# Performance work log

Hardware: AMD Instinct MI355X
Metric: run time of the kernel (lower is better)

The kernel has to match this reference:

```python
import jax, jax.numpy as jnp
import numpy as np

B, N = 2048, 64
D, H = 64, 256
CARD_V, UNIT_V, ENEMY_V, AT_V, SRC_V, MODE_V, TER_V, SITE_V, SKILL_V = 400, 100, 120, 50, 30, 10, 12, 25, 60
STATE_SC, CE_SC, SITE_SC, ME_SC, ACT_SC = 64, 8, 6, 8, 16
L_HAND, L_UNIT, L_CE, L_SK, L_VS, L_ME, L_TGT = 16, 8, 8, 8, 16, 16, 8
STATE_IN = STATE_SC + 6 * D + (D + CE_SC) + (D + SITE_SC) + (D + ME_SC)  # 662
ACT_IN = 7 * D + ACT_SC  # 464


def setup_inputs() -> dict:
    key = jax.random.key(0)
    ks = iter(jax.random.split(key, 64))
    nrm = lambda shape, s=1.0: jax.random.normal(next(ks), shape, jnp.float32) * s
    ri = lambda shape, hi: jax.random.randint(next(ks), shape, 0, hi, jnp.int32)
    return {
        'state_scalars': nrm((B, STATE_SC)),
        'mode_id': ri((B,), MODE_V), 'terrain_id': ri((B,), TER_V), 'site_type_id': ri((B,), SITE_V),
        'hand_ids': ri((B, L_HAND), CARD_V), 'hand_mask': ri((B, L_HAND), 2),
        'unit_ids': ri((B, L_UNIT), UNIT_V), 'unit_mask': ri((B, L_UNIT), 2),
        'combat_enemy_ids': ri((B, L_CE), ENEMY_V), 'combat_enemy_scalars': nrm((B, L_CE, CE_SC)), 'combat_enemy_mask': ri((B, L_CE), 2),
        'skill_ids': ri((B, L_SK), SKILL_V), 'skill_mask': ri((B, L_SK), 2),
        'visible_site_ids': ri((B, L_VS), SITE_V), 'visible_site_scalars': nrm((B, L_VS, SITE_SC)), 'visible_site_mask': ri((B, L_VS), 2),
        'map_enemy_ids': ri((B, L_ME), ENEMY_V), 'map_enemy_scalars': nrm((B, L_ME, ME_SC)), 'map_enemy_mask': ri((B, L_ME), 2),
        'action_ids': ri((B, N, 6), SRC_V),  # SRC_V=30 is min over the 6 id vocabs -> always in range
        'action_scalars': nrm((B, N, ACT_SC)),
        'target_enemy_ids': ri((B, N, L_TGT), ENEMY_V), 'target_mask': ri((B, N, L_TGT), 2),
        'card_emb': nrm((CARD_V, D), 0.05), 'unit_emb': nrm((UNIT_V, D), 0.05), 'enemy_emb': nrm((ENEMY_V, D), 0.05),
        'action_type_emb': nrm((AT_V, D), 0.05), 'source_emb': nrm((SRC_V, D), 0.05), 'mode_emb': nrm((MODE_V, D), 0.05),
        'terrain_emb': nrm((TER_V, D), 0.05), 'site_emb': nrm((SITE_V, D), 0.05), 'skill_emb': nrm((SKILL_V, D), 0.05),
        'map_site_emb': nrm((SITE_V, D), 0.05),
        'W_s': nrm((STATE_IN, H), 0.02), 'b_s': jnp.zeros((H,), jnp.float32),
        'W_a': nrm((ACT_IN, H), 0.02), 'b_a': jnp.zeros((H,), jnp.float32),
        'W1': nrm((2 * H, H), 0.02), 'b1': jnp.zeros((H,), jnp.float32),
        'W2': nrm((H, 1), 0.02), 'b2': jnp.zeros((1,), jnp.float32),
        'W_v': nrm((H, 1), 0.02), 'b_v': jnp.zeros((1,), jnp.float32),
    }


def masked_mean(x, mask):
    # x: [..., L, D'], mask: [..., L] (0/1). Empty list -> zeros (count clamped to 1).
    m = mask.astype(x.dtype)[..., None]
    s = jnp.sum(x * m, axis=-2)
    c = jnp.maximum(jnp.sum(m, axis=-2), 1.0)
    return s / c


def reference(state_scalars, mode_id, terrain_id, site_type_id, hand_ids, hand_mask,
              unit_ids, unit_mask, combat_enemy_ids, combat_enemy_scalars, combat_enemy_mask,
              skill_ids, skill_mask, visible_site_ids, visible_site_scalars, visible_site_mask,
              map_enemy_ids, map_enemy_scalars, map_enemy_mask, action_ids, action_scalars,
              target_enemy_ids, target_mask, card_emb, unit_emb, enemy_emb, action_type_emb,
              source_emb, mode_emb, terrain_emb, site_emb, skill_emb, map_site_emb,
              W_s, b_s, W_a, b_a, W1, b1, W2, b2, W_v, b_v):
    # ---- state encoding (batched version of encode_state) ----
    hand_pool = masked_mean(card_emb[hand_ids], hand_mask)            # [B, D]
    unit_pool = masked_mean(unit_emb[unit_ids], unit_mask)            # [B, D]
    ce = jnp.concatenate([enemy_emb[combat_enemy_ids], combat_enemy_scalars], axis=-1)
    ce_pool = masked_mean(ce, combat_enemy_mask)                      # [B, D+CE_SC]
    skill_pool = masked_mean(skill_emb[skill_ids], skill_mask)        # [B, D]
    vs = jnp.concatenate([map_site_emb[visible_site_ids], visible_site_scalars], axis=-1)
    vs_pool = masked_mean(vs, visible_site_mask)                      # [B, D+SITE_SC]
    me = jnp.concatenate([enemy_emb[map_enemy_ids], map_enemy_scalars], axis=-1)
    me_pool = masked_mean(me, map_enemy_mask)                         # [B, D+ME_SC]
    state_input = jnp.concatenate([
        state_scalars, mode_emb[mode_id], hand_pool, unit_pool,
        terrain_emb[terrain_id], site_emb[site_type_id],
        ce_pool, skill_pool, vs_pool, me_pool], axis=-1)              # [B, 662]
    state_repr = jnp.tanh(state_input @ W_s + b_s)                    # [B, H]
    # ---- action encoding (batched encode_actions) ----
    tgt_pool = masked_mean(enemy_emb[target_enemy_ids], target_mask)  # [B, N, D]
    action_input = jnp.concatenate([
        action_type_emb[action_ids[..., 0]], source_emb[action_ids[..., 1]],
        card_emb[action_ids[..., 2]], unit_emb[action_ids[..., 3]],
        enemy_emb[action_ids[..., 4]], skill_emb[action_ids[..., 5]],
        tgt_pool, action_scalars], axis=-1)                           # [B, N, 464]
    action_reprs = jnp.tanh(action_input @ W_a + b_a)                 # [B, N, H]
    # ---- scoring + value heads ----
    state_b = jnp.broadcast_to(state_repr[:, None, :], (state_repr.shape[0], action_reprs.shape[1], state_repr.shape[1]))
    combined = jnp.concatenate([state_b, action_reprs], axis=-1)      # [B, N, 2H]
    logits = (jnp.tanh(combined @ W1 + b1) @ W2 + b2)[..., 0]         # [B, N]
    value = (state_repr @ W_v + b_v)[..., 0]                          # [B]
    return logits, value
```

## Files before the change

kernel.cpp:

```cpp
#include <hip/hip_runtime.h>
#include <hip/hip_bf16.h>

#define BB 2048
#define NN 64
#define DD 64
#define HH 256
#define L_HAND 16
#define L_UNIT 8
#define L_CE 8
#define L_SK 8
#define L_VS 16
#define L_ME 16
#define L_TGT 8
#define STATE_SC 64
#define CE_SC 8
#define SITE_SC 6
#define ME_SC 8
#define ACT_SC 16
#define STATE_IN 662
#define ACT_IN 464

#define SROWS 2
#define SK 672
#define SSTRIDE 676

typedef __attribute__((ext_vector_type(8))) short short8;
typedef __attribute__((ext_vector_type(4))) float f32x4;

__device__ __forceinline__ float fast_tanh(float x) {
    float e = __expf(2.0f * x);
    return 1.0f - 2.0f * __builtin_amdgcn_rcpf(e + 1.0f);
}
__device__ __forceinline__ short f2bs(float x) {
    __hip_bfloat16 h = __float2bfloat16(x);
    return *reinterpret_cast<short*>(&h);
}
__device__ __forceinline__ float bs2f(short u) {
    union { unsigned int i; float f; } v;
    v.i = ((unsigned int)(unsigned short)u) << 16;
    return v.f;
}
__device__ __forceinline__ void async_copy16(const void* gsrc, void* ldst) {
    __builtin_amdgcn_global_load_lds(
        (const __attribute__((address_space(1))) unsigned int*)gsrc,
        (__attribute__((address_space(3))) unsigned int*)ldst, 16, 0, 0);
}
__device__ __forceinline__ float sum16_dpp(float v) {
    int x;
    x = __builtin_amdgcn_update_dpp(0, __float_as_int(v), 0x111, 0xf, 0xf, true);
    v += __int_as_float(x);
    x = __builtin_amdgcn_update_dpp(0, __float_as_int(v), 0x112, 0xf, 0xf, true);
    v += __int_as_float(x);
    x = __builtin_amdgcn_update_dpp(0, __float_as_int(v), 0x114, 0xf, 0xf, true);
    v += __int_as_float(x);
    x = __builtin_amdgcn_update_dpp(0, __float_as_int(v), 0x118, 0xf, 0xf, true);
    v += __int_as_float(x);
    return v;
}

#define RO_AT    0
#define RO_SRC   50
#define RO_CARD  80
#define RO_UNIT  480
#define RO_ENEMY 580
#define RO_SKILL 700
#define EMB_ROWS 760

#define T0 (480 * 256)
#define T1 (T0 + 256 * 256)
#define T2 (T1 + EMB_ROWS * 64)
#define T3 (T2 + SK * 256)
#define T4 (T3 + 256 * 256)

__global__ __launch_bounds__(256) void pack_kernel(
    const float* __restrict__ W_a, const float* __restrict__ W1,
    const float* __restrict__ W_s,
    const float* __restrict__ at_emb, const float* __restrict__ src_emb,
    const float* __restrict__ card_emb, const float* __restrict__ unit_emb,
    const float* __restrict__ enemy_emb, const float* __restrict__ skill_emb,
    ushort* __restrict__ WaP, ushort* __restrict__ W1bP, ushort* __restrict__ emb16,
    ushort* __restrict__ WsP, ushort* __restrict__ W1aP)
{
    const int idx = blockIdx.x * 256 + threadIdx.x;
    if (idx < T0) {
        const int k = idx >> 8, n = idx & 255;
        const float v = (k < ACT_IN) ? W_a[k * HH + n] : 0.f;
        const int pi = (((k >> 5) * 16 + (n >> 4)) * 64 +
                        ((n & 15) + 16 * ((k >> 3) & 3))) * 8 + (k & 7);
        WaP[pi] = (ushort)f2bs(v);
    } else if (idx < T1) {
        const int j = idx - T0;
        const int k = j >> 8, n = j & 255;
        const float v = W1[(256 + k) * HH + n];
        const int pi = (((k >> 5) * 16 + (n >> 4)) * 64 +
                        ((n & 15) + 16 * ((k >> 3) & 3))) * 8 + (k & 7);
        W1bP[pi] = (ushort)f2bs(v);
    } else if (idx < T2) {
        const int j = idx - T1;
        const int row = j >> 6, d = j & 63;
        float v;
        if      (row < RO_SRC)   v = at_emb[row * 64 + d];
        else if (row < RO_CARD)  v = src_emb[(row - RO_SRC) * 64 + d];
        else if (row < RO_UNIT)  v = card_emb[(row - RO_CARD) * 64 + d];
        else if (row < RO_ENEMY) v = unit_emb[(row - RO_UNIT) * 64 + d];
        else if (row < RO_SKILL) v = enemy_emb[(row - RO_ENEMY) * 64 + d];
        else                     v = skill_emb[(row - RO_SKILL) * 64 + d];
        emb16[j] = (ushort)f2bs(v);
    } else if (idx < T3) {
        const int j = idx - T2;
        const int k = j >> 8, n = j & 255;
        const float v = (k < STATE_IN) ? W_s[k * HH + n] : 0.f;
        const int pi = (((k >> 5) * 16 + (n >> 4)) * 64 +
                        ((n & 15) + 16 * ((k >> 3) & 3))) * 8 + (k & 7);
        WsP[pi] = (ushort)f2bs(v);
    } else if (idx < T4) {
        const int j = idx - T3;
        const int k = j >> 8, n = j & 255;
        const float v = W1[k * HH + n];
        const int pi = (((k >> 5) * 16 + (n >> 4)) * 64 +
                        ((n & 15) + 16 * ((k >> 3) & 3))) * 8 + (k & 7);
        W1aP[pi] = (ushort)f2bs(v);
    }
}

__global__ __launch_bounds__(256) void state_mfma_kernel(
    const float* __restrict__ state_scalars,
    const int* __restrict__ mode_id, const int* __restrict__ terrain_id,
    const int* __restrict__ site_type_id,
    const int* __restrict__ hand_ids, const int* __restrict__ hand_mask,
    const int* __restrict__ unit_ids, const int* __restrict__ unit_mask,
    const int* __restrict__ ce_ids, const float* __restrict__ ce_sc, const int* __restrict__ ce_mask,
    const int* __restrict__ skill_ids, const int* __restrict__ skill_mask,
    const int* __restrict__ vs_ids, const float* __restrict__ vs_sc, const int* __restrict__ vs_mask,
    const int* __restrict__ me_ids, const float* __restrict__ me_sc, const int* __restrict__ me_mask,
    const float* __restrict__ mode_emb, const float* __restrict__ ter_emb,
    const float* __restrict__ site_emb, const float* __restrict__ msite_emb,
    const ushort* __restrict__ emb16,
    const ushort* __restrict__ WsP, const float* __restrict__ b_s,
    const ushort* __restrict__ W1aP,
    const float* __restrict__ W_v, const float* __restrict__ b_v,
    float* __restrict__ s_part, float* __restrict__ out_value)
{
    __shared__ float s_in[SROWS * SSTRIDE];
    __shared__ ushort sA2[8 * 64 * 8];
    __shared__ float red[4][4];

    const int t = threadIdx.x;
    const int b0 = blockIdx.x * SROWS;
    const int w = t >> 6;
    const int lane = t & 63;
    const ushort* card16  = emb16 + RO_CARD  * 64;
    const ushort* unit16  = emb16 + RO_UNIT  * 64;
    const ushort* enemy16 = emb16 + RO_ENEMY * 64;
    const ushort* skill16 = emb16 + RO_SKILL * 64;

    for (int u = t; u < SROWS * 84; u += 256) {
        const int r  = u / 84;
        const int un = u - r * 84;
        const int b  = b0 + r;
        float* dst = s_in + r * SSTRIDE;
        if (un < 8) {
            const int o0 = un * 8;
            const float4 f0 = *(const float4*)(state_scalars + b * STATE_SC + o0);
            const float4 f1 = *(const float4*)(state_scalars + b * STATE_SC + o0 + 4);
            *(float4*)(dst + o0) = f0; *(float4*)(dst + o0 + 4) = f1;
        } else if (un < 16) {
            const int d0 = (un - 8) * 8;
            const float4 f0 = *(const float4*)(mode_emb + mode_id[b] * DD + d0);
            const float4 f1 = *(const float4*)(mode_emb + mode_id[b] * DD + d0 + 4);
            *(float4*)(dst + 64 + d0) = f0; *(float4*)(dst + 64 + d0 + 4) = f1;
        } else if (un < 24) {
            const int d0 = (un - 16) * 8;
            float acc[8] = {0,0,0,0,0,0,0,0}; int c = 0;
#pragma unroll
            for (int l = 0; l < L_HAND; ++l) {
                const int mk = hand_mask[b * L_HAND + l]; c += mk;
                const float fm = (float)mk;
                const short8 e = *(const short8*)(card16 + hand_ids[b * L_HAND + l] * 64 + d0);
#pragma unroll
                for (int q = 0; q < 8; ++q) acc[q] = fmaf(fm, bs2f(e[q]), acc[q]);
            }
            const float inv = 1.0f / (float)(c > 1 ? c : 1);
#pragma unroll
            for (int q = 0; q < 8; ++q) dst[128 + d0 + q] = acc[q] * inv;
        } else if (un < 32) {
            const int d0 = (un - 24) * 8;
            float acc[8] = {0,0,0,0,0,0,0,0}; int c = 0;
#pragma unroll
            for (int l = 0; l < L_UNIT; ++l) {
                const int mk = unit_mask[b * L_UNIT + l]; c += mk;
                const float fm = (float)mk;
                const short8 e = *(const short8*)(unit16 + unit_ids[b * L_UNIT + l] * 64 + d0);
#pragma unroll
                for (int q = 0; q < 8; ++q) acc[q] = fmaf(fm, bs2f(e[q]), acc[q]);
            }
            const float inv = 1.0f / (float)(c > 1 ? c : 1);
#pragma unroll
            for (int q = 0; q < 8; ++q) dst[192 + d0 + q] = acc[q] * inv;
        } else if (un < 40) {
            const int d0 = (un - 32) * 8;
            const float4 f0 = *(const float4*)(ter_emb + terrain_id[b] * DD + d0);
            const float4 f1 = *(const float4*)(ter_emb + terrain_id[b] * DD + d0 + 4);
            *(float4*)(dst + 256 + d0) = f0; *(float4*)(dst + 256 + d0 + 4) = f1;
        } else if (un < 48) {
            const int d0 = (un - 40) * 8;
            const float4 f0 = *(const float4*)(site_emb + site_type_id[b] * DD + d0);
            const float4 f1 = *(const float4*)(site_emb + site_type_id[b] * DD + d0 + 4);
            *(float4*)(dst + 320 + d0) = f0; *(float4*)(dst + 320 + d0 + 4) = f1;
        } else if (un < 56) {
            const int d0 = (un - 48) * 8;
            float acc[8] = {0,0,0,0,0,0,0,0}; int c = 0;
#pragma unroll
            for (int l = 0; l < L_CE; ++l) {
                const int mk = ce_mask[b * L_CE + l]; c += mk;
                const float fm = (float)mk;
                const short8 e = *(const short8*)(enemy16 + ce_ids[b * L_CE + l] * 64 + d0);
#pragma unroll
                for (int q = 0; q < 8; ++q) acc[q] = fmaf(fm, bs2f(e[q]), acc[q]);
            }
            const float inv = 1.0f / (float)(c > 1 ? c : 1);
#pragma unroll
            for (int q = 0; q < 8; ++q) dst[384 + d0 + q] = acc[q] * inv;
        } else if (un == 56) {
            float acc[8] = {0,0,0,0,0,0,0,0}; int c = 0;
#pragma unroll
            for (int l = 0; l < L_CE; ++l) {
                const int mk = ce_mask[b * L_CE + l]; c += mk;
                const float fm = (float)mk;
                const float4 f0 = *(const float4*)(ce_sc + (b * L_CE + l) * CE_SC);
                const float4 f1 = *(const float4*)(ce_sc + (b * L_CE + l) * CE_SC + 4);
                acc[0] = fmaf(fm, f0.x, acc[0]); acc[1] = fmaf(fm, f0.y, acc[1]);
                acc[2] = fmaf(fm, f0.z, acc[2]); acc[3] = fmaf(fm, f0.w, acc[3]);
                acc[4] = fmaf(fm, f1.x, acc[4]); acc[5] = fmaf(fm, f1.y, acc[5]);
                acc[6] = fmaf(fm, f1.z, acc[6]); acc[7] = fmaf(fm, f1.w, acc[7]);
            }
            const float inv = 1.0f / (float)(c > 1 ? c : 1);
#pragma unroll
            for (int q = 0; q < 8; ++q) dst[448 + q] = acc[q] * inv;
        } else if (un < 65) {
            const int d0 = (un - 57) * 8;
            float acc[8] = {0,0,0,0,0,0,0,0}; int c = 0;
#pragma unroll
            for (int l = 0; l < L_SK; ++l) {
                const int mk = skill_mask[b * L_SK + l]; c += mk;
                const float fm = (float)mk;
                const short8 e = *(const short8*)(skill16 + skill_ids[b * L_SK + l] * 64 + d0);
#pragma unroll
                for (int q = 0; q < 8; ++q) acc[q] = fmaf(fm, bs2f(e[q]), acc[q]);
            }
            const float inv = 1.0f / (float)(c > 1 ? c : 1);
#pragma unroll
            for (int q = 0; q < 8; ++q) dst[456 + d0 + q] = acc[q] * inv;
        } else if (un < 73) {
            const int d0 = (un - 65) * 8;
            float acc[8] = {0,0,0,0,0,0,0,0}; int c = 0;
#pragma unroll
            for (int l = 0; l < L_VS; ++l) {
                const int mk = vs_mask[b * L_VS + l]; c += mk;
                const float fm = (float)mk;
                const float4 f0 = *(const float4*)(msite_emb + vs_ids[b * L_VS + l] * DD + d0);
                const float4 f1 = *(const float4*)(msite_emb + vs_ids[b * L_VS + l] * DD + d0 + 4);
                acc[0] = fmaf(fm, f0.x, acc[0]); acc[1] = fmaf(fm, f0.y, acc[1]);
                acc[2] = fmaf(fm, f0.z, acc[2]); acc[3] = fmaf(fm, f0.w, acc[3]);
                acc[4] = fmaf(fm, f1.x, acc[4]); acc[5] = fmaf(fm, f1.y, acc[5]);
                acc[6] = fmaf(fm, f1.z, acc[6]); acc[7] = fmaf(fm, f1.w, acc[7]);
            }
            const float inv = 1.0f / (float)(c > 1 ? c : 1);
#pragma unroll
            for (int q = 0; q < 8; ++q) dst[520 + d0 + q] = acc[q] * inv;
        } else if (un == 73) {
            float acc[6] = {0,0,0,0,0,0}; int c = 0;
#pragma unroll
            for (int l = 0; l < L_VS; ++l) {
                const int mk = vs_mask[b * L_VS + l]; c += mk;
                const float fm = (float)mk;
                const float* p = vs_sc + (b * L_VS + l) * SITE_SC;
#pragma unroll
                for (int q = 0; q < 6; ++q) acc[q] = fmaf(fm, p[q], acc[q]);
            }
            const float inv = 1.0f / (float)(c > 1 ? c : 1);
#pragma unroll
            for (int q = 0; q < 6; ++q) dst[584 + q] = acc[q] * inv;
        } else if (un < 82) {
            const int d0 = (un - 74) * 8;
            float acc[8] = {0,0,0,0,0,0,0,0}; int c = 0;
#pragma unroll
            for (int l = 0; l < L_ME; ++l) {
                const int mk = me_mask[b * L_ME + l]; c += mk;
                const float fm = (float)mk;
                const short8 e = *(const short8*)(enemy16 + me_ids[b * L_ME + l] * 64 + d0);
#pragma unroll
                for (int q = 0; q < 8; ++q) acc[q] = fmaf(fm, bs2f(e[q]), acc[q]);
            }
            const float inv = 1.0f / (float)(c > 1 ? c : 1);
#pragma unroll
            for (int q = 0; q < 8; ++q) dst[590 + d0 + q] = acc[q] * inv;
        } else if (un == 82) {
            float acc[8] = {0,0,0,0,0,0,0,0}; int c = 0;
#pragma unroll
            for (int l = 0; l < L_ME; ++l) {
                const int mk = me_mask[b * L_ME + l]; c += mk;
                const float fm = (float)mk;
                const float4 f0 = *(const float4*)(me_sc + (b * L_ME + l) * ME_SC);
                const float4 f1 = *(const float4*)(me_sc + (b * L_ME + l) * ME_SC + 4);
                acc[0] = fmaf(fm, f0.x, acc[0]); acc[1] = fmaf(fm, f0.y, acc[1]);
                acc[2] = fmaf(fm, f0.z, acc[2]); acc[3] = fmaf(fm, f0.w, acc[3]);
                acc[4] = fmaf(fm, f1.x, acc[4]); acc[5] = fmaf(fm, f1.y, acc[5]);
                acc[6] = fmaf(fm, f1.z, acc[6]); acc[7] = fmaf(fm, f1.w, acc[7]);
            }
            const float inv = 1.0f / (float)(c > 1 ? c : 1);
#pragma unroll
            for (int q = 0; q < 8; ++q) dst[654 + q] = acc[q] * inv;
        } else {
#pragma unroll
            for (int q = 0; q < 10; ++q) dst[662 + q] = 0.f;
        }
    }
    __syncthreads();

    const short8* Ws8  = (const short8*)WsP;
    const short8* W1a8 = (const short8*)W1aP;
    const f32x4 zero = {0.f, 0.f, 0.f, 0.f};
    const int m15 = lane & 15;
    const int g = lane >> 4;
    const float* arow = s_in + (m15 & (SROWS - 1)) * SSTRIDE;

    f32x4 acc1[4];
#pragma unroll
    for (int nt = 0; nt < 4; ++nt) acc1[nt] = zero;

    for (int kt = 0; kt < 21; ++kt) {
        const int k0 = kt * 32 + 8 * g;
        const float4 v0 = *(const float4*)(arow + k0);
        const float4 v1 = *(const float4*)(arow + k0 + 4);
        short8 a;
        a[0] = f2bs(v0.x); a[1] = f2bs(v0.y); a[2] = f2bs(v0.z); a[3] = f2bs(v0.w);
        a[4] = f2bs(v1.x); a[5] = f2bs(v1.y); a[6] = f2bs(v1.z); a[7] = f2bs(v1.w);
        short8 bfr[4];
#pragma unroll
        for (int nt = 0; nt < 4; ++nt) bfr[nt] = Ws8[(kt * 16 + w * 4 + nt) * 64 + lane];
#pragma unroll
        for (int nt = 0; nt < 4; ++nt)
            acc1[nt] = __builtin_amdgcn_mfma_f32_16x16x32_bf16(a, bfr[nt], acc1[nt], 0, 0, 0);
    }

    float sr[4][4];
    float pv[4] = {0.f, 0.f, 0.f, 0.f};
#pragma unroll
    for (int nt = 0; nt < 4; ++nt) {
        const int n = w * 64 + nt * 16 + m15;
        const float bsn = b_s[n];
        const float wvn = W_v[n];
#pragma unroll
        for (int r = 0; r < 4; ++r) {
            const float sv = fast_tanh(acc1[nt][r] + bsn);
            sr[nt][r] = sv;
            pv[r] = fmaf(sv, wvn, pv[r]);
        }
    }
#pragma unroll
    for (int r = 0; r < SROWS; ++r) {
        float v = pv[r];
        v += __shfl_xor(v, 1);
        v += __shfl_xor(v, 2);
        v += __shfl_xor(v, 4);
        v += __shfl_xor(v, 8);
        if (lane == 0) red[w][r] = v;
    }
    if (g == 0) {
#pragma unroll
        for (int nt = 0; nt < 4; ++nt) {
            const int n = w * 64 + nt * 16 + m15;
            const int kt2 = n >> 5;
            const int lo16 = (n >> 3) & 3;
#pragma unroll
            for (int r = 0; r < 4; ++r) {
                const int pi = (kt2 * 64 + (r + 16 * lo16)) * 8 + (n & 7);
                sA2[pi] = (ushort)f2bs(sr[nt][r]);
            }
        }
    }
    __syncthreads();

    if (t < SROWS) {
        out_value[b0 + t] = red[0][t] + red[1][t] + red[2][t] + red[3][t] + b_v[0];
    }

    const short8* sA2_8 = (const short8*)sA2;
    f32x4 acc2[4];
#pragma unroll
    for (int nt = 0; nt < 4; ++nt) acc2[nt] = zero;
#pragma unroll
    for (int kt = 0; kt < 8; ++kt) {
        const short8 a2 = sA2_8[kt * 64 + lane];
        short8 bfr[4];
#pragma unroll
        for (int nt = 0; nt < 4; ++nt) bfr[nt] = W1a8[(kt * 16 + w * 4 + nt) * 64 + lane];
#pragma unroll
        for (int nt = 0; nt < 4; ++nt)
            acc2[nt] = __builtin_amdgcn_mfma_f32_16x16x32_bf16(a2, bfr[nt], acc2[nt], 0, 0, 0);
    }
    if (g == 0) {
#pragma unroll
        for (int nt = 0; nt < 4; ++nt) {
            const int n = w * 64 + nt * 16 + m15;
#pragma unroll
            for (int r = 0; r < SROWS; ++r)
                s_part[(b0 + r) * HH + n] = acc2[nt][r];
        }
    }
}

__device__ __forceinline__ short8 tail_chunk(
    int k0, int m, int b,
    const int* __restrict__ s_tid, const int* __restrict__ s_tmk,
    const ushort* __restrict__ emb16, const float* __restrict__ action_scalars)
{
    short8 val;
    if (k0 < 448) {
        const int d = k0 - 384;
        const ushort* enemy16 = emb16 + RO_ENEMY * 64;
        float accq[8] = {0.f, 0.f, 0.f, 0.f, 0.f, 0.f, 0.f, 0.f};
        int c = 0;
#pragma unroll
        for (int l = 0; l < L_TGT; ++l) {
            const int mk = s_tmk[m * 8 + l];
            c += mk;
            const float fm = (float)mk;
            const short8 e = *(const short8*)(enemy16 + s_tid[m * 8 + l] * 64 + d);
#pragma unroll
            for (int q = 0; q < 8; ++q) accq[q] = fmaf(fm, bs2f(e[q]), accq[q]);
        }
        const float inv = 1.0f / (float)(c > 1 ? c : 1);
#pragma unroll
        for (int q = 0; q < 8; ++q) val[q] = f2bs(accq[q] * inv);
    } else if (k0 < 464) {
        const float* sc = action_scalars + (b * NN + m) * ACT_SC + (k0 - 448);
        const float4 f0 = *(const float4*)sc;
        const float4 f1 = *(const float4*)(sc + 4);
        val[0] = f2bs(f0.x); val[1] = f2bs(f0.y); val[2] = f2bs(f0.z); val[3] = f2bs(f0.w);
        val[4] = f2bs(f1.x); val[5] = f2bs(f1.y); val[6] = f2bs(f1.z); val[7] = f2bs(f1.w);
    } else {
#pragma unroll
        for (int q = 0; q < 8; ++q) val[q] = 0;
    }
    return val;
}

__global__ __launch_bounds__(512) void action_mfma_kernel(
    const int* __restrict__ action_ids, const float* __restrict__ action_scalars,
    const int* __restrict__ tgt_ids, const int* __restrict__ tgt_mask,
    const ushort* __restrict__ emb16,
    const ushort* __restrict__ WaP, const float* __restrict__ b_a,
    const ushort* __restrict__ W1bP, const float* __restrict__ b1,
    const float* __restrict__ W2, const float* __restrict__ b2,
    const float* __restrict__ s_part, float* __restrict__ out_logits)
{
    __shared__ ushort sA[11 * 2048];
    __shared__ float red[8][64];
    __shared__ int s_ids[64 * 6];
    __shared__ int s_tid[64 * 8];
    __shared__ int s_tmk[64 * 8];

    const int t = threadIdx.x;
    const int b = blockIdx.x;
    const int w = t >> 6;
    const int lane = t & 63;
    const int m15 = lane & 15;

    const short8* sA8  = (const short8*)sA;
    short8* sA8w = (short8*)sA;
    const short8* Wa8  = (const short8*)WaP;
    const short8* W1b8 = (const short8*)W1bP;
    const f32x4 zero = {0.f, 0.f, 0.f, 0.f};

    short8 bn0 = Wa8[(w * 2 + 0) * 64 + lane];
    short8 bn1 = Wa8[(w * 2 + 1) * 64 + lane];

    for (int i = t; i < 64 * 6; i += 512) s_ids[i] = action_ids[b * (64 * 6) + i];
    for (int i = t; i < 64 * 8; i += 512) {
        s_tid[i] = tgt_ids[b * (64 * 8) + i];
        s_tmk[i] = tgt_mask[b * (64 * 8) + i];
    }
    __syncthreads();

    const int ROFFS[6] = {RO_AT, RO_SRC, RO_CARD, RO_UNIT, RO_ENEMY, RO_SKILL};

    {
        const int kt = w;
        const int j = kt >> 1;
        const int roff = ROFFS[j];
        const int koff = (kt & 1) * 32 + (lane >> 4) * 8;
#pragma unroll
        for (int i = 0; i < 4; ++i) {
            const int id = s_ids[(i * 16 + m15) * 6 + j];
            const ushort* src = emb16 + (roff + id) * 64 + koff;
            async_copy16(src, sA + kt * 2048 + i * 512);
        }
    }

    {
        const int m = lane;
        const int mt_b = m >> 4, mrow = m & 15;
        for (int kc = 48 + w; kc < 60; kc += 8) {
            const int k0 = kc << 3;
            const short8 val = tail_chunk(k0, m, b, s_tid, s_tmk, emb16, action_scalars);
            const int ktl = (k0 >> 5) - 4;
            const int lo = kc & 3;
            sA8w[(ktl * 4 + mt_b) * 64 + mrow + 16 * lo] = val;
        }
    }
    __syncthreads();

    float ba[2];
#pragma unroll
    for (int nt = 0; nt < 2; ++nt) ba[nt] = b_a[w * 32 + nt * 16 + m15];

    f32x4 acc[4][2];
#pragma unroll
    for (int i = 0; i < 4; ++i) { acc[i][0] = zero; acc[i][1] = zero; }

#pragma unroll
    for (int kt = 0; kt < 8; ++kt) {
        const short8 b0 = bn0, b1 = bn1;
        const int nkt = (kt < 7) ? kt + 1 : 12;
        bn0 = Wa8[(nkt * 16 + w * 2 + 0) * 64 + lane];
        bn1 = Wa8[(nkt * 16 + w * 2 + 1) * 64 + lane];
        short8 a[4];
#pragma unroll
        for (int mti = 0; mti < 4; ++mti) a[mti] = sA8[(kt * 4 + mti) * 64 + lane];
        __builtin_amdgcn_s_setprio(1);
#pragma unroll
        for (int mti = 0; mti < 4; ++mti) {
            acc[mti][0] = __builtin_amdgcn_mfma_f32_16x16x32_bf16(a[mti], b0, acc[mti][0], 0, 0, 0);
            acc[mti][1] = __builtin_amdgcn_mfma_f32_16x16x32_bf16(a[mti], b1, acc[mti][1], 0, 0, 0);
        }
        __builtin_amdgcn_s_setprio(0);
    }
    __syncthreads();

    if (w < 4) {
        const int kt = 8 + w;
        const int j = kt >> 1;
        const int roff = ROFFS[j];
        const int koff = (kt & 1) * 32 + (lane >> 4) * 8;
#pragma unroll
        for (int i = 0; i < 4; ++i) {
            const int id = s_ids[(i * 16 + m15) * 6 + j];
            const ushort* src = emb16 + (roff + id) * 64 + koff;
            async_copy16(src, sA + (kt - 8) * 2048 + i * 512);
        }
    }

#pragma unroll
    for (int kt = 12; kt < 15; ++kt) {
        const short8 b0 = bn0, b1 = bn1;
        const int nkt = (kt < 14) ? kt + 1 : 8;
        bn0 = Wa8[(nkt * 16 + w * 2 + 0) * 64 + lane];
        bn1 = Wa8[(nkt * 16 + w * 2 + 1) * 64 + lane];
        short8 a[4];
#pragma unroll
        for (int mti = 0; mti < 4; ++mti) a[mti] = sA8[((kt - 4) * 4 + mti) * 64 + lane];
        __builtin_amdgcn_s_setprio(1);
#pragma unroll
        for (int mti = 0; mti < 4; ++mti) {
            acc[mti][0] = __builtin_amdgcn_mfma_f32_16x16x32_bf16(a[mti], b0, acc[mti][0], 0, 0, 0);
            acc[mti][1] = __builtin_amdgcn_mfma_f32_16x16x32_bf16(a[mti], b1, acc[mti][1], 0, 0, 0);
        }
        __builtin_amdgcn_s_setprio(0);
    }
    __syncthreads();

    short8 cn0, cn1;
#pragma unroll
    for (int kt = 8; kt < 12; ++kt) {
        const short8 b0 = bn0, b1 = bn1;
        if (kt < 11) {
            bn0 = Wa8[((kt + 1) * 16 + w * 2 + 0) * 64 + lane];
            bn1 = Wa8[((kt + 1) * 16 + w * 2 + 1) * 64 + lane];
        } else {
            cn0 = W1b8[(w * 2 + 0) * 64 + lane];
            cn1 = W1b8[(w * 2 + 1) * 64 + lane];
        }
        short8 a[4];
#pragma unroll
        for (int mti = 0; mti < 4; ++mti) a[mti] = sA8[((kt - 8) * 4 + mti) * 64 + lane];
        __builtin_amdgcn_s_setprio(1);
#pragma unroll
        for (int mti = 0; mti < 4; ++mti) {
            acc[mti][0] = __builtin_amdgcn_mfma_f32_16x16x32_bf16(a[mti], b0, acc[mti][0], 0, 0, 0);
            acc[mti][1] = __builtin_amdgcn_mfma_f32_16x16x32_bf16(a[mti], b1, acc[mti][1], 0, 0, 0);
        }
        __builtin_amdgcn_s_setprio(0);
    }
    __syncthreads();

#pragma unroll
    for (int mti = 0; mti < 4; ++mti)
#pragma unroll
        for (int nt = 0; nt < 2; ++nt) {
            const int n = w * 32 + nt * 16 + m15;
            const int kt2 = n >> 5;
            const int lo16 = (n >> 3) & 3;
#pragma unroll
            for (int r = 0; r < 4; ++r) {
                const int mm = mti * 16 + (lane >> 4) * 4 + r;
                const float h = fast_tanh(acc[mti][nt][r] + ba[nt]);
                const int pi = ((kt2 * 4 + mti) * 64 + ((mm & 15) + 16 * lo16)) * 8 + (n & 7);
                sA[pi] = (ushort)f2bs(h);
            }
        }
    __syncthreads();

    float sp[2], w2v[2];
#pragma unroll
    for (int nt = 0; nt < 2; ++nt) {
        const int n = w * 32 + nt * 16 + m15;
        sp[nt]  = s_part[b * HH + n] + b1[n];
        w2v[nt] = W2[n];
    }

#pragma unroll
    for (int i = 0; i < 4; ++i) { acc[i][0] = zero; acc[i][1] = zero; }

#pragma unroll
    for (int kt = 0; kt < 8; ++kt) {
        const short8 b0 = cn0, b1 = cn1;
        if (kt < 7) {
            cn0 = W1b8[((kt + 1) * 16 + w * 2 + 0) * 64 + lane];
            cn1 = W1b8[((kt + 1) * 16 + w * 2 + 1) * 64 + lane];
        }
        short8 a[4];
#pragma unroll
        for (int mti = 0; mti < 4; ++mti) a[mti] = sA8[(kt * 4 + mti) * 64 + lane];
        __builtin_amdgcn_s_setprio(1);
#pragma unroll
        for (int mti = 0; mti < 4; ++mti) {
            acc[mti][0] = __builtin_amdgcn_mfma_f32_16x16x32_bf16(a[mti], b0, acc[mti][0], 0, 0, 0);
            acc[mti][1] = __builtin_amdgcn_mfma_f32_16x16x32_bf16(a[mti], b1, acc[mti][1], 0, 0, 0);
        }
        __builtin_amdgcn_s_setprio(0);
    }

    float part[4][4];
#pragma unroll
    for (int mti = 0; mti < 4; ++mti)
#pragma unroll
        for (int r = 0; r < 4; ++r) part[mti][r] = 0.f;

#pragma unroll
    for (int mti = 0; mti < 4; ++mti)
#pragma unroll
        for (int nt = 0; nt < 2; ++nt)
#pragma unroll
            for (int r = 0; r < 4; ++r)
                part[mti][r] += fast_tanh(acc[mti][nt][r] + sp[nt]) * w2v[nt];

#pragma unroll
    for (int mti = 0; mti < 4; ++mti)
#pragma unroll
        for (int r = 0; r < 4; ++r)
            part[mti][r] = sum16_dpp(part[mti][r]);

    if (m15 == 15) {
#pragma unroll
        for (int mti = 0; mti < 4; ++mti)
#pragma unroll
            for (int r = 0; r < 4; ++r) {
                const int mm = mti * 16 + (lane >> 4) * 4 + r;
                red[w][mm] = part[mti][r];
            }
    }
    __syncthreads();
    if (t < 64) {
        float s = b2[0];
#pragma unroll
        for (int wi = 0; wi < 8; ++wi) s += red[wi][t];
        out_logits[b * NN + t] = s;
    }
}

extern "C" void kernel_launch(void* const* d_in, const int* in_sizes, int n_in,
                              void* d_out, int out_size, void* d_ws, size_t ws_size,
                              hipStream_t stream) {
    const float* state_scalars = (const float*)d_in[0];
    const int*   mode_id       = (const int*)d_in[1];
    const int*   terrain_id    = (const int*)d_in[2];
    const int*   site_type_id  = (const int*)d_in[3];
    const int*   hand_ids      = (const int*)d_in[4];
    const int*   hand_mask     = (const int*)d_in[5];
    const int*   unit_ids      = (const int*)d_in[6];
    const int*   unit_mask     = (const int*)d_in[7];
    const int*   ce_ids        = (const int*)d_in[8];
    const float* ce_sc         = (const float*)d_in[9];
    const int*   ce_mask       = (const int*)d_in[10];
    const int*   skill_ids     = (const int*)d_in[11];
    const int*   skill_mask    = (const int*)d_in[12];
    const int*   vs_ids        = (const int*)d_in[13];
    const float* vs_sc         = (const float*)d_in[14];
    const int*   vs_mask       = (const int*)d_in[15];
    const int*   me_ids        = (const int*)d_in[16];
    const float* me_sc         = (const float*)d_in[17];
    const int*   me_mask       = (const int*)d_in[18];
    const int*   action_ids    = (const int*)d_in[19];
    const float* action_scalars= (const float*)d_in[20];
    const int*   tgt_ids       = (const int*)d_in[21];
    const int*   tgt_mask      = (const int*)d_in[22];
    const float* card_emb      = (const float*)d_in[23];
    const float* unit_emb      = (const float*)d_in[24];
    const float* enemy_emb     = (const float*)d_in[25];
    const float* at_emb        = (const float*)d_in[26];
    const float* src_emb       = (const float*)d_in[27];
    const float* mode_emb      = (const float*)d_in[28];
    const float* ter_emb       = (const float*)d_in[29];
    const float* site_emb      = (const float*)d_in[30];
    const float* skill_emb     = (const float*)d_in[31];
    const float* msite_emb     = (const float*)d_in[32];
    const float* W_s           = (const float*)d_in[33];
    const float* b_s           = (const float*)d_in[34];
    const float* W_a           = (const float*)d_in[35];
    const float* b_a           = (const float*)d_in[36];
    const float* W1            = (const float*)d_in[37];
    const float* b1            = (const float*)d_in[38];
    const float* W2            = (const float*)d_in[39];
    const float* b2            = (const float*)d_in[40];
    const float* W_v           = (const float*)d_in[41];
    const float* b_v           = (const float*)d_in[42];

    float* out_logits = (float*)d_out;
    float* out_value  = (float*)d_out + (size_t)BB * NN;

    char* ws = (char*)d_ws;
    float*  s_part = (float*)ws;
    ushort* WaP    = (ushort*)(ws + 2097152);
    ushort* W1bP   = (ushort*)(ws + 2342912);
    ushort* emb16  = (ushort*)(ws + 2473984);
    ushort* WsP    = (ushort*)(ws + 2571264);
    ushort* W1aP   = (ushort*)(ws + 2915328);

    pack_kernel<<<(T4 + 255) / 256, 256, 0, stream>>>(
        W_a, W1, W_s, at_emb, src_emb, card_emb, unit_emb, enemy_emb, skill_emb,
        WaP, W1bP, emb16, WsP, W1aP);

    state_mfma_kernel<<<BB / SROWS, 256, 0, stream>>>(
        state_scalars, mode_id, terrain_id, site_type_id,
        hand_ids, hand_mask, unit_ids, unit_mask,
        ce_ids, ce_sc, ce_mask, skill_ids, skill_mask,
        vs_ids, vs_sc, vs_mask, me_ids, me_sc, me_mask,
        mode_emb, ter_emb, site_emb, msite_emb, emb16,
        WsP, b_s, W1aP, W_v, b_v, s_part, out_value);

    action_mfma_kernel<<<BB, 512, 0, stream>>>(
        action_ids, action_scalars, tgt_ids, tgt_mask,
        emb16, WaP, b_a, W1bP, b1, W2, b2, s_part, out_logits);
}
```

Before: 111.3 us.

## Fuse state encoder into per-batch action kernel, dropping s_part round trip

Merges the state-encoding kernel into the action kernel so each 512-thread block computes its own state row, value head and W1 state partial in shared memory instead of going through a global s_part buffer and a separate launch. Target ids and masks are now read directly from global memory inside tail_chunk rather than staged in shared memory. This removes one launch and the global write/read of the state partial. In exchange, each block runs 16-row MFMAs for a single useful row, which wastes most of the state-path matrix work compared with the previous 2-rows-per-block layout.

New measurement: 170.3 us. +53.0%, slower.

```diff
diff --git a/kernel.cpp b/kernel.cpp
--- a/kernel.cpp
+++ b/kernel.cpp
@@ -19,10 +19,7 @@
 #define ACT_SC 16
 #define STATE_IN 662
 #define ACT_IN 464
-
-#define SROWS 2
 #define SK 672
-#define SSTRIDE 676
 
 typedef __attribute__((ext_vector_type(8))) short short8;
 typedef __attribute__((ext_vector_type(4))) float f32x4;
@@ -123,7 +120,50 @@
     }
 }
 
-__global__ __launch_bounds__(256) void state_mfma_kernel(
+__device__ __forceinline__ short8 tail_chunk(
+    int k0, int m, int b,
+    const int* __restrict__ tgt_ids, const int* __restrict__ tgt_mask,
+    const ushort* __restrict__ emb16, const float* __restrict__ action_scalars)
+{
+    short8 val;
+    if (k0 < 448) {
+        const int d = k0 - 384;
+        const ushort* enemy16 = emb16 + RO_ENEMY * 64;
+        const int base = (b * NN + m) * L_TGT;
+        const int4 t0v = *(const int4*)(tgt_ids + base);
+        const int4 t1v = *(const int4*)(tgt_ids + base + 4);
+        const int4 m0v = *(const int4*)(tgt_mask + base);
+        const int4 m1v = *(const int4*)(tgt_mask + base + 4);
+        const int tid[8] = {t0v.x, t0v.y, t0v.z, t0v.w, t1v.x, t1v.y, t1v.z, t1v.w};
+        const int tmk[8] = {m0v.x, m0v.y, m0v.z, m0v.w, m1v.x, m1v.y, m1v.z, m1v.w};
+        float accq[8] = {0.f, 0.f, 0.f, 0.f, 0.f, 0.f, 0.f, 0.f};
+        int c = 0;
+#pragma unroll
+        for (int l = 0; l < L_TGT; ++l) {
+            const int mk = tmk[l];
+            c += mk;
+            const float fm = (float)mk;
+            const short8 e = *(const short8*)(enemy16 + tid[l] * 64 + d);
+#pragma unroll
+            for (int q = 0; q < 8; ++q) accq[q] = fmaf(fm, bs2f(e[q]), accq[q]);
+        }
+        const float inv = 1.0f / (float)(c > 1 ? c : 1);
+#pragma unroll
+        for (int q = 0; q < 8; ++q) val[q] = f2bs(accq[q] * inv);
+    } else if (k0 < 464) {
+        const float* sc = action_scalars + (b * NN + m) * ACT_SC + (k0 - 448);
+        const float4 f0 = *(const float4*)sc;
+        const float4 f1 = *(const float4*)(sc + 4);
+        val[0] = f2bs(f0.x); val[1] = f2bs(f0.y); val[2] = f2bs(f0.z); val[3] = f2bs(f0.w);
+        val[4] = f2bs(f1.x); val[5] = f2bs(f1.y); val[6] = f2bs(f1.z); val[7] = f2bs(f1.w);
+    } else {
+#pragma unroll
+        for (int q = 0; q < 8; ++q) val[q] = 0;
+    }
+    return val;
+}
+
+__global__ __launch_bounds__(512) void fused_mfma_kernel(
     const float* __restrict__ state_scalars,
     const int* __restrict__ mode_id, const int* __restrict__ terrain_id,
     const int* __restrict__ site_type_id,
@@ -135,30 +175,49 @@
     const int* __restrict__ me_ids, const float* __restrict__ me_sc, const int* __restrict__ me_mask,
     const float* __restrict__ mode_emb, const float* __restrict__ ter_emb,
     const float* __restrict__ site_emb, const float* __restrict__ msite_emb,
+    const int* __restrict__ action_ids, const float* __restrict__ action_scalars,
+    const int* __restrict__ tgt_ids, const int* __restrict__ tgt_mask,
     const ushort* __restrict__ emb16,
+    const ushort* __restrict__ WaP, const float* __restrict__ b_a,
+    const ushort* __restrict__ W1bP, const float* __restrict__ b1,
+    const float* __restrict__ W2, const float* __restrict__ bias2,
     const ushort* __restrict__ WsP, const float* __restrict__ b_s,
     const ushort* __restrict__ W1aP,
     const float* __restrict__ W_v, const float* __restrict__ b_v,
-    float* __restrict__ s_part, float* __restrict__ out_value)
+    float* __restrict__ out_logits, float* __restrict__ out_value)
 {
-    __shared__ float s_in[SROWS * SSTRIDE];
-    __shared__ ushort sA2[8 * 64 * 8];
-    __shared__ float red[4][4];
+    __shared__ ushort sA[11 * 2048];
+    __shared__ float red[8][64];
+    __shared__ int s_ids[64 * 6];
+    __shared__ float s_in[680];
+    __shared__ float sSP[256];
+    __shared__ ushort sRepr[256];
 
     const int t = threadIdx.x;
-    const int b0 = blockIdx.x * SROWS;
+    const int b = blockIdx.x;
     const int w = t >> 6;
     const int lane = t & 63;
+    const int m15 = lane & 15;
+
+    const short8* sA8  = (const short8*)sA;
+    short8* sA8w = (short8*)sA;
+    const short8* Wa8  = (const short8*)WaP;
+    const short8* W1b8 = (const short8*)W1bP;
+    const short8* Ws8  = (const short8*)WsP;
+    const short8* W1a8 = (const short8*)W1aP;
+    const f32x4 zero = {0.f, 0.f, 0.f, 0.f};
+
     const ushort* card16  = emb16 + RO_CARD  * 64;
     const ushort* unit16  = emb16 + RO_UNIT  * 64;
     const ushort* enemy16 = emb16 + RO_ENEMY * 64;
     const ushort* skill16 = emb16 + RO_SKILL * 64;
 
-    for (int u = t; u < SROWS * 84; u += 256) {
-        const int r  = u / 84;
-        const int un = u - r * 84;
-        const int b  = b0 + r;
-        float* dst = s_in + r * SSTRIDE;
+    short8 bn0 = Wa8[(w * 2 + 0) * 64 + lane];
+    short8 bn1 = Wa8[(w * 2 + 1) * 64 + lane];
+
+    if (t < 84) {
+        const int un = t;
+        float* dst = s_in;
         if (un < 8) {
             const int o0 = un * 8;
             const float4 f0 = *(const float4*)(state_scalars + b * STATE_SC + o0);
@@ -316,172 +375,8 @@
             for (int q = 0; q < 10; ++q) dst[662 + q] = 0.f;
         }
     }
-    __syncthreads();
-
-    const short8* Ws8  = (const short8*)WsP;
-    const short8* W1a8 = (const short8*)W1aP;
-    const f32x4 zero = {0.f, 0.f, 0.f, 0.f};
-    const int m15 = lane & 15;
-    const int g = lane >> 4;
-    const float* arow = s_in + (m15 & (SROWS - 1)) * SSTRIDE;
-
-    f32x4 acc1[4];
-#pragma unroll
-    for (int nt = 0; nt < 4; ++nt) acc1[nt] = zero;
-
-    for (int kt = 0; kt < 21; ++kt) {
-        const int k0 = kt * 32 + 8 * g;
-        const float4 v0 = *(const float4*)(arow + k0);
-        const float4 v1 = *(const float4*)(arow + k0 + 4);
-        short8 a;
-        a[0] = f2bs(v0.x); a[1] = f2bs(v0.y); a[2] = f2bs(v0.z); a[3] = f2bs(v0.w);
-        a[4] = f2bs(v1.x); a[5] = f2bs(v1.y); a[6] = f2bs(v1.z); a[7] = f2bs(v1.w);
-        short8 bfr[4];
-#pragma unroll
-        for (int nt = 0; nt < 4; ++nt) bfr[nt] = Ws8[(kt * 16 + w * 4 + nt) * 64 + lane];
-#pragma unroll
-        for (int nt = 0; nt < 4; ++nt)
-            acc1[nt] = __builtin_amdgcn_mfma_f32_16x16x32_bf16(a, bfr[nt], acc1[nt], 0, 0, 0);
-    }
-
-    float sr[4][4];
-    float pv[4] = {0.f, 0.f, 0.f, 0.f};
-#pragma unroll
-    for (int nt = 0; nt < 4; ++nt) {
-        const int n = w * 64 + nt * 16 + m15;
-        const float bsn = b_s[n];
-        const float wvn = W_v[n];
-#pragma unroll
-        for (int r = 0; r < 4; ++r) {
-            const float sv = fast_tanh(acc1[nt][r] + bsn);
-            sr[nt][r] = sv;
-            pv[r] = fmaf(sv, wvn, pv[r]);
-        }
-    }
-#pragma unroll
-    for (int r = 0; r < SROWS; ++r) {
-        float v = pv[r];
-        v += __shfl_xor(v, 1);
-        v += __shfl_xor(v, 2);
-        v += __shfl_xor(v, 4);
-        v += __shfl_xor(v, 8);
-        if (lane == 0) red[w][r] = v;
-    }
-    if (g == 0) {
-#pragma unroll
-        for (int nt = 0; nt < 4; ++nt) {
-            const int n = w * 64 + nt * 16 + m15;
-            const int kt2 = n >> 5;
-            const int lo16 = (n >> 3) & 3;
-#pragma unroll
-            for (int r = 0; r < 4; ++r) {
-                const int pi = (kt2 * 64 + (r + 16 * lo16)) * 8 + (n & 7);
-                sA2[pi] = (ushort)f2bs(sr[nt][r]);
-            }
-        }
-    }
-    __syncthreads();
-
-    if (t < SROWS) {
-        out_value[b0 + t] = red[0][t] + red[1][t] + red[2][t] + red[3][t] + b_v[0];
-    }
-
-    const short8* sA2_8 = (const short8*)sA2;
-    f32x4 acc2[4];
-#pragma unroll
-    for (int nt = 0; nt < 4; ++nt) acc2[nt] = zero;
-#pragma unroll
-    for (int kt = 0; kt < 8; ++kt) {
-        const short8 a2 = sA2_8[kt * 64 + lane];
-        short8 bfr[4];
-#pragma unroll
-        for (int nt = 0; nt < 4; ++nt) bfr[nt] = W1a8[(kt * 16 + w * 4 + nt) * 64 + lane];
-#pragma unroll
-        for (int nt = 0; nt < 4; ++nt)
-            acc2[nt] = __builtin_amdgcn_mfma_f32_16x16x32_bf16(a2, bfr[nt], acc2[nt], 0, 0, 0);
-    }
-    if (g == 0) {
-#pragma unroll
-        for (int nt = 0; nt < 4; ++nt) {
-            const int n = w * 64 + nt * 16 + m15;
-#pragma unroll
-            for (int r = 0; r < SROWS; ++r)
-                s_part[(b0 + r) * HH + n] = acc2[nt][r];
-        }
-    }
-}
-
-__device__ __forceinline__ short8 tail_chunk(
-    int k0, int m, int b,
-    const int* __restrict__ s_tid, const int* __restrict__ s_tmk,
-    const ushort* __restrict__ emb16, const float* __restrict__ action_scalars)
-{
-    short8 val;
-    if (k0 < 448) {
-        const int d = k0 - 384;
-        const ushort* enemy16 = emb16 + RO_ENEMY * 64;
-        float accq[8] = {0.f, 0.f, 0.f, 0.f, 0.f, 0.f, 0.f, 0.f};
-        int c = 0;
-#pragma unroll
-        for (int l = 0; l < L_TGT; ++l) {
-            const int mk = s_tmk[m * 8 + l];
-            c += mk;
-            const float fm = (float)mk;
-            const short8 e = *(const short8*)(enemy16 + s_tid[m * 8 + l] * 64 + d);
-#pragma unroll
-            for (int q = 0; q < 8; ++q) accq[q] = fmaf(fm, bs2f(e[q]), accq[q]);
-        }
-        const float inv = 1.0f / (float)(c > 1 ? c : 1);
-#pragma unroll
-        for (int q = 0; q < 8; ++q) val[q] = f2bs(accq[q] * inv);
-    } else if (k0 < 464) {
-        const float* sc = action_scalars + (b * NN + m) * ACT_SC + (k0 - 448);
-        const float4 f0 = *(const float4*)sc;
-        const float4 f1 = *(const float4*)(sc + 4);
-        val[0] = f2bs(f0.x); val[1] = f2bs(f0.y); val[2] = f2bs(f0.z); val[3] = f2bs(f0.w);
-        val[4] = f2bs(f1.x); val[5] = f2bs(f1.y); val[6] = f2bs(f1.z); val[7] = f2bs(f1.w);
-    } else {
-#pragma unroll
-        for (int q = 0; q < 8; ++q) val[q] = 0;
-    }
-    return val;
-}
-
-__global__ __launch_bounds__(512) void action_mfma_kernel(
-    const int* __restrict__ action_ids, const float* __restrict__ action_scalars,
-    const int* __restrict__ tgt_ids, const int* __restrict__ tgt_mask,
-    const ushort* __restrict__ emb16,
-    const ushort* __restrict__ WaP, const float* __restrict__ b_a,
-    const ushort* __restrict__ W1bP, const float* __restrict__ b1,
-    const float* __restrict__ W2, const float* __restrict__ b2,
-    const float* __restrict__ s_part, float* __restrict__ out_logits)
-{
-    __shared__ ushort sA[11 * 2048];
-    __shared__ float red[8][64];
-    __shared__ int s_ids[64 * 6];
-    __shared__ int s_tid[64 * 8];
-    __shared__ int s_tmk[64 * 8];
-
-    const int t = threadIdx.x;
-    const int b = blockIdx.x;
-    const int w = t >> 6;
-    const int lane = t & 63;
-    const int m15 = lane & 15;
-
-    const short8* sA8  = (const short8*)sA;
-    short8* sA8w = (short8*)sA;
-    const short8* Wa8  = (const short8*)WaP;
-    const short8* W1b8 = (const short8*)W1bP;
-    const f32x4 zero = {0.f, 0.f, 0.f, 0.f};
-
-    short8 bn0 = Wa8[(w * 2 + 0) * 64 + lane];
-    short8 bn1 = Wa8[(w * 2 + 1) * 64 + lane];
 
     for (int i = t; i < 64 * 6; i += 512) s_ids[i] = action_ids[b * (64 * 6) + i];
-    for (int i = t; i < 64 * 8; i += 512) {
-        s_tid[i] = tgt_ids[b * (64 * 8) + i];
-        s_tmk[i] = tgt_mask[b * (64 * 8) + i];
-    }
     __syncthreads();
 
     const int ROFFS[6] = {RO_AT, RO_SRC, RO_CARD, RO_UNIT, RO_ENEMY, RO_SKILL};
@@ -504,7 +399,7 @@
         const int mt_b = m >> 4, mrow = m & 15;
         for (int kc = 48 + w; kc < 60; kc += 8) {
             const int k0 = kc << 3;
-            const short8 val = tail_chunk(k0, m, b, s_tid, s_tmk, emb16, action_scalars);
+            const short8 val = tail_chunk(k0, m, b, tgt_ids, tgt_mask, emb16, action_scalars);
             const int ktl = (k0 >> 5) - 4;
             const int lo = kc & 3;
             sA8w[(ktl * 4 + mt_b) * 64 + mrow + 16 * lo] = val;
@@ -569,7 +464,52 @@
         }
         __builtin_amdgcn_s_setprio(0);
     }
+
+    {
+        f32x4 sacc0 = zero, sacc1 = zero;
+        short8 sn0 = Ws8[(w * 2 + 0) * 64 + lane];
+        short8 sn1 = Ws8[(w * 2 + 1) * 64 + lane];
+        for (int kt = 0; kt < 21; ++kt) {
+            const short8 wb0 = sn0, wb1 = sn1;
+            if (kt < 20) {
+                sn0 = Ws8[((kt + 1) * 16 + w * 2 + 0) * 64 + lane];
+                sn1 = Ws8[((kt + 1) * 16 + w * 2 + 1) * 64 + lane];
+            }
+            const float* ap = s_in + kt * 32 + 8 * (lane >> 4);
+            const float4 v0 = *(const float4*)ap;
+            const float4 v1 = *(const float4*)(ap + 4);
+            short8 a;
+            a[0] = f2bs(v0.x); a[1] = f2bs(v0.y); a[2] = f2bs(v0.z); a[3] = f2bs(v0.w);
+            a[4] = f2bs(v1.x); a[5] = f2bs(v1.y); a[6] = f2bs(v1.z); a[7] = f2bs(v1.w);
+            sacc0 = __builtin_amdgcn_mfma_f32_16x16x32_bf16(a, wb0, sacc0, 0, 0, 0);
+            sacc1 = __builtin_amdgcn_mfma_f32_16x16x32_bf16(a, wb1, sacc1, 0, 0, 0);
+        }
+        if ((lane >> 4) == 0) {
+            float pv = 0.f;
+            {
+                const int n = w * 32 + m15;
+                const float sv = fast_tanh(sacc0[0] + b_s[n]);
+                sRepr[n] = (ushort)f2bs(sv);
+                pv = fmaf(sv, W_v[n], pv);
+            }
+            {
+                const int n = w * 32 + 16 + m15;
+                const float sv = fast_tanh(sacc1[0] + b_s[n]);
+                sRepr[n] = (ushort)f2bs(sv);
+                pv = fmaf(sv, W_v[n], pv);
+            }
+            pv = sum16_dpp(pv);
+            if (m15 == 15) red[w][0] = pv;
+        }
+    }
     __syncthreads();
+
+    if (t == 0) {
+        float s = b_v[0];
+#pragma unroll
+        for (int wi = 0; wi < 8; ++wi) s += red[wi][0];
+        out_value[b] = s;
+    }
 
     short8 cn0, cn1;
 #pragma unroll
@@ -593,6 +533,27 @@
         }
         __builtin_amdgcn_s_setprio(0);
     }
+
+    {
+        f32x4 pacc0 = zero, pacc1 = zero;
+        short8 pn0 = W1a8[(w * 2 + 0) * 64 + lane];
+        short8 pn1 = W1a8[(w * 2 + 1) * 64 + lane];
+#pragma unroll
+        for (int kt = 0; kt < 8; ++kt) {
+            const short8 wb0 = pn0, wb1 = pn1;
+            if (kt < 7) {
+                pn0 = W1a8[((kt + 1) * 16 + w * 2 + 0) * 64 + lane];
+                pn1 = W1a8[((kt + 1) * 16 + w * 2 + 1) * 64 + lane];
+            }
+            const short8 a2 = *(const short8*)(sRepr + kt * 32 + 8 * (lane >> 4));
+            pacc0 = __builtin_amdgcn_mfma_f32_16x16x32_bf16(a2, wb0, pacc0, 0, 0, 0);
+            pacc1 = __builtin_amdgcn_mfma_f32_16x16x32_bf16(a2, wb1, pacc1, 0, 0, 0);
+        }
+        if ((lane >> 4) == 0) {
+            sSP[w * 32 + m15] = pacc0[0];
+            sSP[w * 32 + 16 + m15] = pacc1[0];
+        }
+    }
     __syncthreads();
 
 #pragma unroll
@@ -616,7 +577,7 @@
 #pragma unroll
     for (int nt = 0; nt < 2; ++nt) {
         const int n = w * 32 + nt * 16 + m15;
-        sp[nt]  = s_part[b * HH + n] + b1[n];
+        sp[nt]  = sSP[n] + b1[n];
         w2v[nt] = W2[n];
     }
 
@@ -673,7 +634,7 @@
     }
     __syncthreads();
     if (t < 64) {
-        float s = b2[0];
+        float s = bias2[0];
 #pragma unroll
         for (int wi = 0; wi < 8; ++wi) s += red[wi][t];
         out_logits[b * NN + t] = s;
@@ -731,26 +692,24 @@
     float* out_value  = (float*)d_out + (size_t)BB * NN;
 
     char* ws = (char*)d_ws;
-    float*  s_part = (float*)ws;
-    ushort* WaP    = (ushort*)(ws + 2097152);
-    ushort* W1bP   = (ushort*)(ws + 2342912);
-    ushort* emb16  = (ushort*)(ws + 2473984);
-    ushort* WsP    = (ushort*)(ws + 2571264);
-    ushort* W1aP   = (ushort*)(ws + 2915328);
+    ushort* WaP    = (ushort*)(ws + 0);
+    ushort* W1bP   = (ushort*)(ws + 245760);
+    ushort* emb16  = (ushort*)(ws + 376832);
+    ushort* WsP    = (ushort*)(ws + 474112);
+    ushort* W1aP   = (ushort*)(ws + 818176);
 
     pack_kernel<<<(T4 + 255) / 256, 256, 0, stream>>>(
         W_a, W1, W_s, at_emb, src_emb, card_emb, unit_emb, enemy_emb, skill_emb,
         WaP, W1bP, emb16, WsP, W1aP);
 
-    state_mfma_kernel<<<BB / SROWS, 256, 0, stream>>>(
+    fused_mfma_kernel<<<BB, 512, 0, stream>>>(
         state_scalars, mode_id, terrain_id, site_type_id,
         hand_ids, hand_mask, unit_ids, unit_mask,
         ce_ids, ce_sc, ce_mask, skill_ids, skill_mask,
         vs_ids, vs_sc, vs_mask, me_ids, me_sc, me_mask,
-        mode_emb, ter_emb, site_emb, msite_emb, emb16,
-        WsP, b_s, W1aP, W_v, b_v, s_part, out_value);
-
-    action_mfma_kernel<<<BB, 512, 0, stream>>>(
+        mode_emb, ter_emb, site_emb, msite_emb,
         action_ids, action_scalars, tgt_ids, tgt_mask,
-        emb16, WaP, b_a, W1bP, b1, W2, b2, s_part, out_logits);
-}
+        emb16, WaP, b_a, W1bP, b1, W2, b2,
+        WsP, b_s, W1aP, W_v, b_v,
+        out_logits, out_value);
+}
```
